# Kernel tuning notes

Measured on AMD Instinct MI355X. Metric: run time of the kernel, lower is better.

The kernel has to match this reference:

```python
import jax, jax.numpy as jnp
import numpy as np

B, S, V, E, P, C = 256, 128, 32000, 300, 200, 3
DIST_CUTOFF = 10

def _seq_mask(x):
    # TF: count_nonzero over seq, sequence_mask, expand to [B, S, 1]
    size = jnp.sum(x != 0, axis=1)
    m = (jnp.arange(S)[None, :] < size[:, None]).astype(jnp.float32)
    return m[:, :, None]

def _l2norm(w):
    n = jnp.sqrt(jnp.maximum(jnp.sum(w * w, axis=-1, keepdims=True), 1e-12))
    return w / n

def setup_inputs() -> dict:
    key = jax.random.key(0)
    ks = jax.random.split(key, 11)
    std = 0.01
    x1 = jax.random.randint(ks[0], (B, S), 0, V, dtype=jnp.int32)
    x2 = jax.random.randint(ks[1], (B, S), 0, V, dtype=jnp.int32)
    emb = jax.random.normal(ks[2], (V, E), jnp.float32)
    w_intra = jax.random.normal(ks[3], (E, E), jnp.float32) * std
    bias_intra = jax.random.normal(ks[4], (1,), jnp.float32) * std
    w_proj1 = jax.random.normal(ks[5], (2 * E, P), jnp.float32) * std
    w_proj2 = jax.random.normal(ks[6], (2 * E, P), jnp.float32) * std
    w_att = jax.random.normal(ks[7], (P, P), jnp.float32) * std
    w_cmp1 = jax.random.normal(ks[8], (2 * P, 2 * P), jnp.float32) * std
    w_cmp2 = jax.random.normal(ks[9], (2 * P, 2 * P), jnp.float32) * std
    w_agg = jax.random.normal(ks[10], (4 * P, C), jnp.float32) * std
    return dict(x1=x1, x2=x2, emb=emb, w_intra=w_intra, bias_intra=bias_intra,
                w_proj1=w_proj1, w_proj2=w_proj2, w_att=w_att,
                w_cmp1=w_cmp1, w_cmp2=w_cmp2, w_agg=w_agg)

def reference(x1, x2, emb, w_intra, bias_intra, w_proj1, w_proj2, w_att, w_cmp1, w_cmp2, w_agg):
    relu = jax.nn.relu
    mask1, mask2 = _seq_mask(x1), _seq_mask(x2)  # [B,S,1]

    # normalized embedding lookup
    e = _l2norm(emb)
    e1, e2 = e[x1], e[x2]  # [B,S,E]

    # intra-attention with distance bias (bias zeroed for |i-j| < 10)
    idx = jnp.arange(S)
    dist = jnp.abs(idx[None, :] - idx[:, None])
    dbias = bias_intra[0] * (dist >= DIST_CUTOFF).astype(jnp.float32)  # [S,S]

    def intra(x):
        f = relu(x @ w_intra)                       # shared F, [B,S,E]
        att = jnp.einsum('bik,bjk->bij', f, f)      # [B,S,S]
        sm = jax.nn.softmax(att + dbias[None], axis=2)
        xp = jnp.einsum('bik,bkj->bij', sm, x)
        return jnp.concatenate([x, xp], axis=2)     # [B,S,2E]

    e1, e2 = intra(e1), intra(e2)

    # project
    x1p = relu(e1 @ w_proj1)  # [B,S,P]
    x2p = relu(e2 @ w_proj2)

    # attend: F(x1) . F(x2), multiplicative mask, two softmaxes
    f1 = relu(x1p @ w_att)
    f2 = relu(x2p @ w_att)
    sim = jnp.einsum('bik,bjk->bij', f1, f2)          # [B,S1,S2]
    sim = sim * (mask1 * jnp.swapaxes(mask2, 1, 2))   # multiplicative mask (as in source)
    alpha = jnp.einsum('bki,bkj->bij', jax.nn.softmax(sim, axis=1), x1p)  # [B,S2,P]
    beta = jnp.einsum('bik,bkj->bij', jax.nn.softmax(sim, axis=2), x2p)   # [B,S1,P]

    # compare
    v1 = relu(jnp.concatenate([x1p, beta], axis=2) @ w_cmp1)
    v2 = relu(jnp.concatenate([x2p, alpha], axis=2) @ w_cmp2)

    # aggregate (masked sum pooling) + final ReLU projection (faithful to source)
    v1 = jnp.sum(v1 * mask1, axis=1)
    v2 = jnp.sum(v2 * mask2, axis=1)
    y_hat = relu(jnp.concatenate([v1, v2], axis=1) @ w_agg)  # [B,C]
    return y_hat
```

## Files before the change

kernel.cpp:

```cpp
#include <hip/hip_runtime.h>

#define BATCH 256
#define SEQ   128
#define EDIM  300
#define PDIM  200
#define BSTOK (BATCH * SEQ)

#define F_RELU  1
#define F_ACCUM 2

typedef unsigned short u16;
typedef __attribute__((ext_vector_type(8))) short bf16x8;
typedef __attribute__((ext_vector_type(4))) float f32x4;

__device__ __forceinline__ u16 f2bf(float x) {
    unsigned u = __float_as_uint(x);
    unsigned r = u + 0x7fffu + ((u >> 16) & 1u);
    return (u16)(r >> 16);
}
__device__ __forceinline__ float bf2f(u16 h) {
    return __uint_as_float(((unsigned)h) << 16);
}

__device__ __forceinline__ unsigned char* swz16(unsigned char* base, int row, int chunk) {
    return base + row * 64 + (((chunk ^ (row >> 1)) & 3) << 4);
}

__device__ __forceinline__ void split_store_swz(const float* va,
    unsigned char* bH, unsigned char* bL, int row, int c0)
{
    unsigned hp[8], lp[8];
    #pragma unroll
    for (int i = 0; i < 8; i++) {
        const unsigned u0 = __float_as_uint(va[2 * i]);
        const unsigned u1 = __float_as_uint(va[2 * i + 1]);
        const unsigned h0 = u0 & 0xffff0000u;
        const unsigned h1 = u1 & 0xffff0000u;
        hp[i] = (u0 >> 16) | h1;
        const float r0 = va[2 * i]     - __uint_as_float(h0);
        const float r1 = va[2 * i + 1] - __uint_as_float(h1);
        lp[i] = (__float_as_uint(r0) >> 16) | (__float_as_uint(r1) & 0xffff0000u);
    }
    *(uint4*)swz16(bH, row, c0)     = make_uint4(hp[0], hp[1], hp[2], hp[3]);
    *(uint4*)swz16(bH, row, c0 + 1) = make_uint4(hp[4], hp[5], hp[6], hp[7]);
    *(uint4*)swz16(bL, row, c0)     = make_uint4(lp[0], lp[1], lp[2], lp[3]);
    *(uint4*)swz16(bL, row, c0 + 1) = make_uint4(lp[4], lp[5], lp[6], lp[7]);
}

__device__ __forceinline__ void hi_store_swz(const float* va,
    unsigned char* bH, int row, int c0)
{
    unsigned hp[8];
    #pragma unroll
    for (int i = 0; i < 8; i++)
        hp[i] = (unsigned)f2bf(va[2 * i]) | ((unsigned)f2bf(va[2 * i + 1]) << 16);
    *(uint4*)swz16(bH, row, c0)     = make_uint4(hp[0], hp[1], hp[2], hp[3]);
    *(uint4*)swz16(bH, row, c0 + 1) = make_uint4(hp[4], hp[5], hp[6], hp[7]);
}

__device__ __forceinline__ void gload16(float* va, const float* __restrict__ src,
                                        bool row_ok)
{
    if (row_ok) {
        #pragma unroll
        for (int i = 0; i < 4; i++) {
            const float4 v = *(const float4*)(src + i * 4);
            va[i * 4 + 0] = v.x; va[i * 4 + 1] = v.y;
            va[i * 4 + 2] = v.z; va[i * 4 + 3] = v.w;
        }
    } else {
        #pragma unroll
        for (int i = 0; i < 16; i++) va[i] = 0.f;
    }
}

__device__ __forceinline__ void kmask16(float* va, int kbase, int Kvalid)
{
    #pragma unroll
    for (int i = 0; i < 16; i++)
        va[i] = (kbase + i < Kvalid) ? va[i] : 0.f;
}

__device__ __forceinline__ void gload_emb(float* va, const float* __restrict__ erow,
                                          int kb)
{
    if (kb + 16 <= EDIM) {
        #pragma unroll
        for (int i = 0; i < 4; i++) {
            const float4 v = *(const float4*)(erow + kb + i * 4);
            va[i * 4 + 0] = v.x; va[i * 4 + 1] = v.y;
            va[i * 4 + 2] = v.z; va[i * 4 + 3] = v.w;
        }
    } else {
        #pragma unroll
        for (int i = 0; i < 16; i++)
            va[i] = (kb + i < EDIM) ? erow[kb + i] : 0.f;
    }
}

#define MFMA3(ai, aj) \
    acc[ai][aj] = __builtin_amdgcn_mfma_f32_16x16x32_bf16(fah[ai], fbh[aj], acc[ai][aj], 0, 0, 0); \
    acc[ai][aj] = __builtin_amdgcn_mfma_f32_16x16x32_bf16(fah[ai], fbl[aj], acc[ai][aj], 0, 0, 0); \
    acc[ai][aj] = __builtin_amdgcn_mfma_f32_16x16x32_bf16(fal[ai], fbh[aj], acc[ai][aj], 0, 0, 0);

#define MFMA1(ai, aj) \
    acc[ai][aj] = __builtin_amdgcn_mfma_f32_16x16x32_bf16(fah[ai], fbh[aj], acc[ai][aj], 0, 0, 0);

__device__ __forceinline__ void store_transposed(
    float* __restrict__ PT, const f32x4 (*acc)[4], float* TR,
    int bn, int Nvalid, int wm, int wn, int lr, int quad, int tid, bool relu)
{
    #pragma unroll
    for (int h = 0; h < 2; h++) {
        __syncthreads();
        if ((wn >> 6) == h) {
            #pragma unroll
            for (int j = 0; j < 4; j++) {
                const int col = j * 16 + lr;
                #pragma unroll
                for (int i = 0; i < 4; i++)
                    #pragma unroll
                    for (int r = 0; r < 4; r++) {
                        float v = acc[i][j][r];
                        if (relu) v = fmaxf(v, 0.f);
                        TR[col * 129 + wm + i * 16 + quad * 4 + r] = v;
                    }
            }
        }
        __syncthreads();
        const int row = tid >> 2;
        const int gp = bn + h * 64 + row;
        if (gp < Nvalid) {
            float* dst = PT + (long long)gp * 128;
            for (int c = (tid & 3); c < 32; c += 4) {
                const int base = row * 129 + c * 4;
                *(float4*)(dst + c * 4) =
                    make_float4(TR[base], TR[base + 1], TR[base + 2], TR[base + 3]);
            }
        }
    }
}

__global__ __launch_bounds__(256) void gemm_proj(
    const int* __restrict__ x1, const int* __restrict__ x2,
    const float* __restrict__ emb, const float* __restrict__ norms,
    const u16* __restrict__ W1h, const u16* __restrict__ W1l,
    const u16* __restrict__ W2h, const u16* __restrict__ W2l,
    float* __restrict__ T, float* __restrict__ F0, float* __restrict__ F1)
{
    __shared__ __align__(16) unsigned char smem[65536];

    const int tid = threadIdx.x;
    const int id  = blockIdx.y * 5 + blockIdx.x;
    const int xcd = id & 7;
    const int s   = id >> 3;
    const int mt  = xcd + 8 * (s / 5);
    const int bm  = mt * 128;
    const int bn  = (s % 5) * 128;
    const bool side2 = mt >= 256;
    const bool wb = bn < 256;

    const u16* Bh = side2 ? W2h : W1h;
    const u16* Bl = side2 ? W2l : W1l;
    float* F = side2 ? F1 : F0;
    const int fm = side2 ? bm - 32768 : bm;
    const int* toks = (side2 ? x2 - 32768 : x1) + bm;

    const int wave = tid >> 6;
    const int lane = tid & 63;
    const int wm   = (wave >> 1) * 64;
    const int wn   = (wave & 1) * 64;
    const int lr   = lane & 15;
    const int quad = lane >> 4;
    const int sr   = tid >> 1;
    const int sc   = (tid & 1) * 16;
    const int c0   = (tid & 1) * 2;

    const int tok = toks[sr];
    const float nrm = norms[tok];
    const float* erow = emb + (long long)tok * EDIM;

    const int gn = bn + sr;
    const bool bok = gn < 556;
    const u16* Bhp = Bh + (long long)gn * 320 + sc;
    const u16* Blp = Bl + (long long)gn * 320 + sc;

    f32x4 acc[4][4];
    #pragma unroll
    for (int i = 0; i < 4; i++)
        #pragma unroll
        for (int j = 0; j < 4; j++)
            acc[i][j] = (f32x4)(0.0f);

    float av[16];
    uint4 bh0, bh1, bl0, bl1;

#define PROJ_LOAD(sidx) do { \
    const int kk_ = (sidx) * 32; \
    gload_emb(av, erow, kk_ + sc); \
    bh0 = bok ? *(const uint4*)(Bhp + kk_)     : make_uint4(0,0,0,0); \
    bh1 = bok ? *(const uint4*)(Bhp + kk_ + 8) : make_uint4(0,0,0,0); \
    if (wb) { \
        bl0 = bok ? *(const uint4*)(Blp + kk_)     : make_uint4(0,0,0,0); \
        bl1 = bok ? *(const uint4*)(Blp + kk_ + 8) : make_uint4(0,0,0,0); \
    } \
} while (0)

#define PROJ_COMMIT(bufp) do { \
    _Pragma("unroll") \
    for (int i_ = 0; i_ < 16; i_++) av[i_] *= nrm; \
    if (wb) split_store_swz(av, (bufp), (bufp) + 8192, sr, c0); \
    else    hi_store_swz(av, (bufp), sr, c0); \
    *(uint4*)swz16((bufp) + 16384, sr, c0)     = bh0; \
    *(uint4*)swz16((bufp) + 16384, sr, c0 + 1) = bh1; \
    if (wb) { \
        *(uint4*)swz16((bufp) + 24576, sr, c0)     = bl0; \
        *(uint4*)swz16((bufp) + 24576, sr, c0 + 1) = bl1; \
    } \
} while (0)

    PROJ_LOAD(0);
    PROJ_COMMIT(smem);
    PROJ_LOAD(1);
    __syncthreads();

    for (int t = 0; t < 10; ++t) {
        unsigned char* rb  = smem + (t & 1) * 32768;
        unsigned char* wbb = smem + ((t & 1) ^ 1) * 32768;

        bf16x8 fah[4], fbh[4];
        #pragma unroll
        for (int i = 0; i < 4; i++) {
            fah[i] = *(const bf16x8*)swz16(rb,         wm + i * 16 + lr, quad);
            fbh[i] = *(const bf16x8*)swz16(rb + 16384, wn + i * 16 + lr, quad);
        }
        if (wb) {
            bf16x8 fal[4], fbl[4];
            #pragma unroll
            for (int i = 0; i < 4; i++) {
                fal[i] = *(const bf16x8*)swz16(rb + 8192,  wm + i * 16 + lr, quad);
                fbl[i] = *(const bf16x8*)swz16(rb + 24576, wn + i * 16 + lr, quad);
            }
            if (t < 9) PROJ_COMMIT(wbb);
            if (t < 8) PROJ_LOAD(t + 2);
            #pragma unroll
            for (int i = 0; i < 4; i++)
                #pragma unroll
                for (int j = 0; j < 4; j++) { MFMA3(i, j) }
        } else {
            if (t < 9) PROJ_COMMIT(wbb);
            if (t < 8) PROJ_LOAD(t + 2);
            #pragma unroll
            for (int i = 0; i < 4; i++)
                #pragma unroll
                for (int j = 0; j < 4; j++) { MFMA1(i, j) }
        }
        __syncthreads();
    }
#undef PROJ_LOAD
#undef PROJ_COMMIT

    if (wb) {
        float* Tb = T + (long long)mt * (PDIM * SEQ);
        store_transposed(Tb, acc, (float*)smem, bn, PDIM, wm, wn, lr, quad, tid, false);
    } else {
        #pragma unroll
        for (int i = 0; i < 4; i++) {
            #pragma unroll
            for (int j = 0; j < 4; j++) {
                const int idx = bn + wn + j * 16 + lr - 256;
                if (idx >= EDIM) continue;
                #pragma unroll
                for (int r = 0; r < 4; r++) {
                    const int gm = fm + wm + i * 16 + quad * 4 + r;
                    F[(long long)gm * EDIM + idx] = fmaxf(acc[i][j][r], 0.f);
                }
            }
        }
    }
}

__global__ __launch_bounds__(256) void gemm_xp(
    const float* __restrict__ P, float* __restrict__ T,
    const int* __restrict__ x1, const int* __restrict__ x2,
    const float* __restrict__ emb, const float* __restrict__ norms,
    const u16* __restrict__ W1h, const u16* __restrict__ W1l,
    const u16* __restrict__ W2h, const u16* __restrict__ W2l,
    float* __restrict__ XCAT)
{
    __shared__ __align__(16) unsigned char smem[65536];

    const int tid = threadIdx.x;
    const int bz  = blockIdx.z;
    const int bn  = blockIdx.x * 128;

    const int wave = tid >> 6;
    const int lane = tid & 63;
    const int wm   = (wave >> 1) * 64;
    const int wn   = (wave & 1) * 64;
    const int lr   = lane & 15;
    const int quad = lane >> 4;
    const int sr   = tid >> 1;
    const int sc   = (tid & 1) * 16;
    const int c0   = (tid & 1) * 2;

    const int* toks = (bz < BATCH) ? x1 + bz * SEQ : x2 + (bz - BATCH) * SEQ;
    const u16* Wh = (bz < BATCH) ? W1h : W2h;
    const u16* Wl = (bz < BATCH) ? W1l : W2l;
    const int tok = toks[sr];
    const float nrm = norms[tok];
    const float* erow = emb + (long long)tok * EDIM;
    const float* Pb = P + (long long)bz * (SEQ * SEQ);
    float* Tb = T + (long long)bz * (PDIM * SEQ);

    const int gn = bn + sr;
    const bool bok = gn < PDIM;
    const u16* Whp = Wh + (long long)gn * 320 + sc;
    const u16* Wlp = Wl + (long long)gn * 320 + sc;
    const float* Pp = Pb + (long long)sr * 128 + sc;
    const float* Tp = Tb + (long long)gn * 128 + sc;

    f32x4 acc[4][4];
    #pragma unroll
    for (int i = 0; i < 4; i++)
        #pragma unroll
        for (int j = 0; j < 4; j++)
            acc[i][j] = (f32x4)(0.0f);

    float av[16], bv[16];
    uint4 bh0, bh1, bl0, bl1;

#define XP_LOAD(sidx) do { \
    if ((sidx) < 10) { \
        const int kk_ = (sidx) * 32; \
        gload_emb(av, erow, kk_ + sc); \
        bh0 = bok ? *(const uint4*)(Whp + kk_)     : make_uint4(0,0,0,0); \
        bh1 = bok ? *(const uint4*)(Whp + kk_ + 8) : make_uint4(0,0,0,0); \
        bl0 = bok ? *(const uint4*)(Wlp + kk_)     : make_uint4(0,0,0,0); \
        bl1 = bok ? *(const uint4*)(Wlp + kk_ + 8) : make_uint4(0,0,0,0); \
    } else { \
        const int kk_ = ((sidx) - 10) * 32; \
        gload16(av, Pp + kk_, true); \
        gload16(bv, Tp + kk_, bok); \
    } \
} while (0)

#define XP_COMMIT(sidx, bufp) do { \
    if ((sidx) < 10) { \
        _Pragma("unroll") \
        for (int i_ = 0; i_ < 16; i_++) av[i_] *= nrm; \
        split_store_swz(av, (bufp), (bufp) + 8192, sr, c0); \
        *(uint4*)swz16((bufp) + 16384, sr, c0)     = bh0; \
        *(uint4*)swz16((bufp) + 16384, sr, c0 + 1) = bh1; \
        *(uint4*)swz16((bufp) + 24576, sr, c0)     = bl0; \
        *(uint4*)swz16((bufp) + 24576, sr, c0 + 1) = bl1; \
    } else { \
        split_store_swz(av, (bufp),         (bufp) + 8192,  sr, c0); \
        split_store_swz(bv, (bufp) + 16384, (bufp) + 24576, sr, c0); \
    } \
} while (0)

    XP_LOAD(0);
    XP_COMMIT(0, smem);
    XP_LOAD(1);
    __syncthreads();

    for (int t = 0; t < 14; ++t) {
        unsigned char* rb  = smem + (t & 1) * 32768;
        unsigned char* wbb = smem + ((t & 1) ^ 1) * 32768;

        bf16x8 fah[4], fal[4], fbh[4], fbl[4];
        #pragma unroll
        for (int i = 0; i < 4; i++) {
            fah[i] = *(const bf16x8*)swz16(rb,         wm + i * 16 + lr, quad);
            fal[i] = *(const bf16x8*)swz16(rb + 8192,  wm + i * 16 + lr, quad);
            fbh[i] = *(const bf16x8*)swz16(rb + 16384, wn + i * 16 + lr, quad);
            fbl[i] = *(const bf16x8*)swz16(rb + 24576, wn + i * 16 + lr, quad);
        }
        if (t < 13) XP_COMMIT(t + 1, wbb);
        if (t < 12) XP_LOAD(t + 2);
        #pragma unroll
        for (int i = 0; i < 4; i++)
            #pragma unroll
            for (int j = 0; j < 4; j++) { MFMA3(i, j) }
        __syncthreads();
    }
#undef XP_LOAD
#undef XP_COMMIT

    const long long rowbase = (long long)bz * SEQ;
    #pragma unroll
    for (int i = 0; i < 4; i++) {
        #pragma unroll
        for (int j = 0; j < 4; j++) {
            const int gnn = bn + wn + j * 16 + lr;
            if (gnn >= PDIM) continue;
            #pragma unroll
            for (int r = 0; r < 4; r++) {
                const int gm = wm + i * 16 + quad * 4 + r;
                XCAT[(rowbase + gm) * 400 + gnn] = fmaxf(acc[i][j][r], 0.f);
            }
        }
    }
    store_transposed(Tb, acc, (float*)smem, bn, PDIM, wm, wn, lr, quad, tid, true);
}

template <int NM>
__global__ __launch_bounds__(256) void gemm_flat(
    const float* __restrict__ A,
    const u16* __restrict__ Bh, const u16* __restrict__ Bl,
    const u16* __restrict__ Bh2, const u16* __restrict__ Bl2, int Msplit,
    float* __restrict__ C, float* __restrict__ PO, const int* __restrict__ sizes,
    int M, int N, int Kp, int lda, int ldb, int ldc, int flags)
{
    constexpr int BUFB = (NM == 3) ? 32768 : 16384;
    constexpr int BOFF = (NM == 3) ? 16384 : 8192;
    __shared__ __align__(16) unsigned char smem[2 * BUFB];

    const int tid = threadIdx.x;
    int bx = blockIdx.x, by = blockIdx.y;
    if ((gridDim.y & 7) == 0) {
        const int gx = gridDim.x;
        const int id = by * gx + bx;
        const int xcd = id & 7;
        const int s = id >> 3;
        by = xcd + 8 * (s / gx);
        bx = s % gx;
    }
    const int bm = by * 128;
    const int bn = bx * 128;

    const int wave = tid >> 6;
    const int lane = tid & 63;
    const int wm   = (wave >> 1) * 64;
    const int wn   = (wave & 1) * 64;
    const int lr   = lane & 15;
    const int quad = lane >> 4;
    const int sr   = tid >> 1;
    const int sc   = (tid & 1) * 16;
    const int c0   = (tid & 1) * 2;

    if (bm >= Msplit) { Bh = Bh2; Bl = Bl2; }

    const float* Ap = A + (long long)(bm + sr) * lda + sc;
    const int gn = bn + sr;
    const bool bok = gn < N;
    const u16* Bhp = Bh + (long long)gn * ldb + sc;
    const u16* Blp = Bl + (long long)gn * ldb + sc;

    f32x4 acc[4][4];
    #pragma unroll
    for (int i = 0; i < 4; i++)
        #pragma unroll
        for (int j = 0; j < 4; j++)
            acc[i][j] = (f32x4)(0.0f);

    float av[16];
    uint4 bh0, bh1, bl0, bl1;

#define FLAT_LOAD(sidx) do { \
    const int kk_ = (sidx) * 32; \
    gload16(av, Ap + kk_, true); \
    bh0 = bok ? *(const uint4*)(Bhp + kk_)     : make_uint4(0,0,0,0); \
    bh1 = bok ? *(const uint4*)(Bhp + kk_ + 8) : make_uint4(0,0,0,0); \
    if constexpr (NM == 3) { \
        bl0 = bok ? *(const uint4*)(Blp + kk_)     : make_uint4(0,0,0,0); \
        bl1 = bok ? *(const uint4*)(Blp + kk_ + 8) : make_uint4(0,0,0,0); \
    } \
} while (0)

#define FLAT_COMMIT(bufp) do { \
    if constexpr (NM == 3) { \
        split_store_swz(av, (bufp), (bufp) + 8192, sr, c0); \
        *(uint4*)swz16((bufp) + BOFF + 8192, sr, c0)     = bl0; \
        *(uint4*)swz16((bufp) + BOFF + 8192, sr, c0 + 1) = bl1; \
    } else { \
        hi_store_swz(av, (bufp), sr, c0); \
    } \
    *(uint4*)swz16((bufp) + BOFF, sr, c0)     = bh0; \
    *(uint4*)swz16((bufp) + BOFF, sr, c0 + 1) = bh1; \
} while (0)

    const int NT = Kp >> 5;
    FLAT_LOAD(0);
    FLAT_COMMIT(smem);
    FLAT_LOAD(1);
    __syncthreads();

    for (int t = 0; t < NT; ++t) {
        unsigned char* rb  = smem + (t & 1) * BUFB;
        unsigned char* wbb = smem + ((t & 1) ^ 1) * BUFB;

        bf16x8 fah[4], fbh[4];
        #pragma unroll
        for (int i = 0; i < 4; i++) {
            fah[i] = *(const bf16x8*)swz16(rb,        wm + i * 16 + lr, quad);
            fbh[i] = *(const bf16x8*)swz16(rb + BOFF, wn + i * 16 + lr, quad);
        }
        if constexpr (NM == 3) {
            bf16x8 fal[4], fbl[4];
            #pragma unroll
            for (int i = 0; i < 4; i++) {
                fal[i] = *(const bf16x8*)swz16(rb + 8192,        wm + i * 16 + lr, quad);
                fbl[i] = *(const bf16x8*)swz16(rb + BOFF + 8192, wn + i * 16 + lr, quad);
            }
            if (t < NT - 1) FLAT_COMMIT(wbb);
            if (t < NT - 2) FLAT_LOAD(t + 2);
            #pragma unroll
            for (int i = 0; i < 4; i++)
                #pragma unroll
                for (int j = 0; j < 4; j++) { MFMA3(i, j) }
        } else {
            if (t < NT - 1) FLAT_COMMIT(wbb);
            if (t < NT - 2) FLAT_LOAD(t + 2);
            #pragma unroll
            for (int i = 0; i < 4; i++)
                #pragma unroll
                for (int j = 0; j < 4; j++) { MFMA1(i, j) }
        }
        __syncthreads();
    }
#undef FLAT_LOAD
#undef FLAT_COMMIT

    const int sz = PO ? sizes[bm >> 7] : 0;
    float ps[4] = {0.f, 0.f, 0.f, 0.f};
    #pragma unroll
    for (int j = 0; j < 4; j++) {
        const int gnn = bn + wn + j * 16 + lr;
        const bool gok = gnn < N;
        #pragma unroll
        for (int i = 0; i < 4; i++) {
            #pragma unroll
            for (int r = 0; r < 4; r++) {
                const int row = wm + i * 16 + quad * 4 + r;
                const int gm = bm + row;
                float v = acc[i][j][r];
                if (flags & F_RELU) v = fmaxf(v, 0.f);
                if (gok && C) C[(long long)gm * ldc + gnn] = v;
                if (PO && row < sz) ps[j] += v;
            }
        }
    }
    if (PO) {
        #pragma unroll
        for (int j = 0; j < 4; j++) {
            ps[j] += __shfl_xor(ps[j], 16);
            ps[j] += __shfl_xor(ps[j], 32);
        }
        float* PS = (float*)smem;
        __syncthreads();
        if (wm == 0 && quad == 0) {
            #pragma unroll
            for (int j = 0; j < 4; j++) PS[wn + j * 16 + lr] = ps[j];
        }
        __syncthreads();
        if (wm == 64 && quad == 0) {
            #pragma unroll
            for (int j = 0; j < 4; j++) PS[wn + j * 16 + lr] += ps[j];
        }
        __syncthreads();
        if (tid < 128) {
            const int gnn = bn + tid;
            if (gnn < N) PO[(long long)(bm >> 7) * N + gnn] = PS[tid];
        }
    }
}

#define SLD 132
template <int MODE>
__global__ __launch_bounds__(256) void gemm_bat(
    const float* __restrict__ A, const float* __restrict__ Aalt,
    const float* __restrict__ B, const float* __restrict__ Balt,
    float* __restrict__ C, float* __restrict__ PT,
    int N, int Kvalid, int Kp, int lda, int ldb, int ldc,
    long long sA, long long sB, long long sC, long long sPT,
    int flags, const float* __restrict__ bias_ptr, const int* __restrict__ sizes,
    int same_ab)
{
    constexpr int NM = (MODE == 0) ? 3 : 1;
    constexpr int BUFB = (NM == 3) ? 32768 : 16384;
    constexpr int BOFF = (NM == 3) ? 16384 : 8192;
    constexpr int SMB  = (MODE == 0) ? 65536 : (128 * SLD * 4);
    __shared__ __align__(16) unsigned char smem[SMB];

    const int bz = blockIdx.z;
    long long zb = bz;
    const float* Ause = A;
    const float* Buse = B;
    if (Aalt && bz >= BATCH) { Ause = Aalt; Buse = Balt; zb = bz - BATCH; }
    Ause += zb * sA;
    Buse += zb * sB;
    C += (long long)bz * sC;
    if (PT) PT += (long long)bz * sPT;

    const int tid  = threadIdx.x;
    const int bn   = blockIdx.x * 128;
    const int wave = tid >> 6;
    const int lane = tid & 63;
    const int wm   = (wave >> 1) * 64;
    const int wn   = (wave & 1) * 64;
    const int lr   = lane & 15;
    const int quad = lane >> 4;
    const int sr   = tid >> 1;
    const int sc   = (tid & 1) * 16;
    const int c0   = (tid & 1) * 2;

    f32x4 acc[4][4];
    #pragma unroll
    for (int i = 0; i < 4; i++)
        #pragma unroll
        for (int j = 0; j < 4; j++)
            acc[i][j] = (f32x4)(0.0f);

    const float* Apt = Ause + (long long)sr * lda + sc;
    const int gn = bn + sr;
    const bool bok = gn < N;
    const float* Bpt = Buse + (long long)gn * ldb + sc;

    float av[16], bv[16];

#define BAT_LOAD(sidx) do { \
    const int kk_ = (sidx) * 32; \
    gload16(av, Apt + kk_, true); \
    if (!same_ab) gload16(bv, Bpt + kk_, bok); \
} while (0)

#define BAT_COMMIT(sidx, bufp) do { \
    kmask16(av, (sidx) * 32 + sc, Kvalid); \
    if constexpr (NM == 3) split_store_swz(av, (bufp), (bufp) + 8192, sr, c0); \
    else                   hi_store_swz(av, (bufp), sr, c0); \
    if (!same_ab) { \
        kmask16(bv, (sidx) * 32 + sc, Kvalid); \
        if constexpr (NM == 3) \
            split_store_swz(bv, (bufp) + BOFF, (bufp) + BOFF + 8192, sr, c0); \
        else \
            hi_store_swz(bv, (bufp) + BOFF, sr, c0); \
    } \
} while (0)

    const int NT = Kp >> 5;
    BAT_LOAD(0);
    BAT_COMMIT(0, smem);
    BAT_LOAD(1);
    __syncthreads();

    for (int t = 0; t < NT; ++t) {
        unsigned char* rb  = smem + (t & 1) * BUFB;
        unsigned char* wbb = smem + ((t & 1) ^ 1) * BUFB;
        unsigned char* rbB = same_ab ? rb : rb + BOFF;

        bf16x8 fah[4], fbh[4];
        #pragma unroll
        for (int i = 0; i < 4; i++) {
            fah[i] = *(const bf16x8*)swz16(rb,  wm + i * 16 + lr, quad);
            fbh[i] = *(const bf16x8*)swz16(rbB, wn + i * 16 + lr, quad);
        }
        if constexpr (NM == 3) {
            bf16x8 fal[4], fbl[4];
            #pragma unroll
            for (int i = 0; i < 4; i++) {
                fal[i] = *(const bf16x8*)swz16(rb + 8192,  wm + i * 16 + lr, quad);
                fbl[i] = *(const bf16x8*)swz16(rbB + 8192, wn + i * 16 + lr, quad);
            }
            if (t < NT - 1) BAT_COMMIT(t + 1, wbb);
            if (t < NT - 2) BAT_LOAD(t + 2);
            #pragma unroll
            for (int i = 0; i < 4; i++)
                #pragma unroll
                for (int j = 0; j < 4; j++) { MFMA3(i, j) }
        } else {
            if (t < NT - 1) BAT_COMMIT(t + 1, wbb);
            if (t < NT - 2) BAT_LOAD(t + 2);
            #pragma unroll
            for (int i = 0; i < 4; i++)
                #pragma unroll
                for (int j = 0; j < 4; j++) { MFMA1(i, j) }
        }
        __syncthreads();
    }
#undef BAT_LOAD
#undef BAT_COMMIT

    if (MODE == 1) {
        float* S = (float*)smem;
        const float bias = bias_ptr[0];
        #pragma unroll
        for (int i = 0; i < 4; i++) {
            #pragma unroll
            for (int j = 0; j < 4; j++) {
                const int col = wn + j * 16 + lr;
                #pragma unroll
                for (int r = 0; r < 4; r++) {
                    const int row = wm + i * 16 + quad * 4 + r;
                    int d = row - col; d = d < 0 ? -d : d;
                    S[row * SLD + col] = acc[i][j][r] + ((d >= 10) ? bias : 0.f);
                }
            }
        }
        __syncthreads();
        const int row = tid >> 1;
        const int half = (tid & 1) * 64;
        float* Sr = S + row * SLD + half;
        float mx = -1e30f;
        #pragma unroll
        for (int c = 0; c < 16; c++) {
            const float4 v = *(const float4*)(Sr + c * 4);
            mx = fmaxf(fmaxf(fmaxf(mx, v.x), fmaxf(v.y, v.z)), v.w);
        }
        mx = fmaxf(mx, __shfl_xor(mx, 1));
        float sum = 0.f;
        #pragma unroll
        for (int c = 0; c < 16; c++) {
            float4 v = *(const float4*)(Sr + c * 4);
            v.x = __expf(v.x - mx); v.y = __expf(v.y - mx);
            v.z = __expf(v.z - mx); v.w = __expf(v.w - mx);
            sum += (v.x + v.y) + (v.z + v.w);
            *(float4*)(Sr + c * 4) = v;
        }
        sum += __shfl_xor(sum, 1);
        const float inv = 1.f / sum;
        #pragma unroll
        for (int c = 0; c < 16; c++) {
            float4 v = *(const float4*)(Sr + c * 4);
            v.x *= inv; v.y *= inv; v.z *= inv; v.w *= inv;
            *(float4*)&C[(long long)row * ldc + half + c * 4] = v;
        }
    } else if (MODE == 2) {
        float* S = (float*)smem;
        const int s1 = sizes[bz];
        const int s2 = sizes[BATCH + bz];
        #pragma unroll
        for (int i = 0; i < 4; i++) {
            #pragma unroll
            for (int j = 0; j < 4; j++) {
                const int col = wn + j * 16 + lr;
                #pragma unroll
                for (int r = 0; r < 4; r++) {
                    const int row = wm + i * 16 + quad * 4 + r;
                    float v = acc[i][j][r];
                    if (row >= s1 || col >= s2) v = 0.f;
                    S[row * SLD + col] = v;
                }
            }
        }
        __syncthreads();
        const int idx = tid >> 1;
        const int half = (tid & 1) * 64;
        {
            const float* Sr = S + idx * SLD + half;
            float mx = -1e30f;
            #pragma unroll
            for (int c = 0; c < 16; c++) {
                const float4 v = *(const float4*)(Sr + c * 4);
                mx = fmaxf(fmaxf(fmaxf(mx, v.x), fmaxf(v.y, v.z)), v.w);
            }
            mx = fmaxf(mx, __shfl_xor(mx, 1));
            float sum = 0.f;
            #pragma unroll
            for (int c = 0; c < 16; c++) {
                const float4 v = *(const float4*)(Sr + c * 4);
                sum += (__expf(v.x - mx) + __expf(v.y - mx))
                     + (__expf(v.z - mx) + __expf(v.w - mx));
            }
            sum += __shfl_xor(sum, 1);
            const float inv = 1.f / sum;
            #pragma unroll
            for (int c = 0; c < 16; c++) {
                const float4 v = *(const float4*)(Sr + c * 4);
                float4 o;
                o.x = __expf(v.x - mx) * inv; o.y = __expf(v.y - mx) * inv;
                o.z = __expf(v.z - mx) * inv; o.w = __expf(v.w - mx) * inv;
                *(float4*)&C[(long long)idx * 128 + half + c * 4] = o;
            }
        }
        {
            float mx = -1e30f;
            for (int r = 0; r < 64; r++)
                mx = fmaxf(mx, S[(half + r) * SLD + idx]);
            mx = fmaxf(mx, __shfl_xor(mx, 1));
            float sum = 0.f;
            for (int r = 0; r < 64; r++)
                sum += __expf(S[(half + r) * SLD + idx] - mx);
            sum += __shfl_xor(sum, 1);
            const float inv = 1.f / sum;
            #pragma unroll
            for (int r4 = 0; r4 < 16; r4++) {
                float4 o;
                o.x = __expf(S[(half + r4 * 4 + 0) * SLD + idx] - mx) * inv;
                o.y = __expf(S[(half + r4 * 4 + 1) * SLD + idx] - mx) * inv;
                o.z = __expf(S[(half + r4 * 4 + 2) * SLD + idx] - mx) * inv;
                o.w = __expf(S[(half + r4 * 4 + 3) * SLD + idx] - mx) * inv;
                *(float4*)&PT[(long long)idx * 128 + half + r4 * 4] = o;
            }
        }
    } else {
        const int s1 = sizes ? sizes[bz] : SEQ;
        const int s2 = sizes ? sizes[BATCH + bz] : SEQ;
        #pragma unroll
        for (int i = 0; i < 4; i++) {
            #pragma unroll
            for (int j = 0; j < 4; j++) {
                const int gnn = bn + wn + j * 16 + lr;
                if (gnn >= N) continue;
                #pragma unroll
                for (int r = 0; r < 4; r++) {
                    const int gm = wm + i * 16 + quad * 4 + r;
                    float v = acc[i][j][r];
                    if (sizes && (gm >= s1 || gnn >= s2)) v = 0.f;
                    if (flags & F_ACCUM) v += C[(long long)gm * ldc + gnn];
                    if (flags & F_RELU)  v = fmaxf(v, 0.f);
                    C[(long long)gm * ldc + gnn] = v;
                    if (PT) PT[(long long)gnn * 128 + gm] = v;
                }
            }
        }
    }
}

struct WEnt { const float* src; u16* H; u16* L; int K, N, Kp, rowStart; };
struct WTab { WEnt e[11]; };
__global__ void convert_all(WTab t)
{
    const int row = blockIdx.y;
    const int k = blockIdx.x * 256 + threadIdx.x;
    #pragma unroll
    for (int s = 0; s < 11; s++) {
        const WEnt w = t.e[s];
        if (row >= w.rowStart && row < w.rowStart + w.N) {
            const int n = row - w.rowStart;
            if (k < w.Kp) {
                const float v = (k < w.K) ? w.src[(long long)k * w.N + n] : 0.f;
                const u16 h = f2bf(v);
                w.H[(long long)n * w.Kp + k] = h;
                w.L[(long long)n * w.Kp + k] = f2bf(v - bf2f(h));
            }
            return;
        }
    }
}

__global__ void norms_kernel(const float* __restrict__ emb, float* __restrict__ norms)
{
    const int r = blockIdx.x;
    const int lane = threadIdx.x;
    const float* row = emb + (long long)r * EDIM;
    float ss = 0.f;
    #pragma unroll
    for (int i = 0; i < 5; i++) {
        const int c = lane + i * 64;
        const float f = (c < EDIM) ? row[c] : 0.f;
        ss += f * f;
    }
    #pragma unroll
    for (int o = 32; o > 0; o >>= 1) ss += __shfl_xor(ss, o);
    if (lane == 0) norms[r] = rsqrtf(fmaxf(ss, 1e-12f));
}

__global__ void sizes_kernel(const int* __restrict__ x1, const int* __restrict__ x2,
                             int* __restrict__ sizes)
{
    const int b = blockIdx.x;
    const int side = blockIdx.y;
    const int* x = (side ? x2 : x1) + b * SEQ;
    const int nz = (x[threadIdx.x] != 0) ? 1 : 0;
    const unsigned long long bal = __ballot(nz);
    __shared__ int part[2];
    if ((threadIdx.x & 63) == 0) part[threadIdx.x >> 6] = __popcll(bal);
    __syncthreads();
    if (threadIdx.x == 0) sizes[side * BATCH + b] = part[0] + part[1];
}

__global__ void agg_kernel(const float* __restrict__ v1s, const float* __restrict__ v2s,
                           const float* __restrict__ w_agg, float* __restrict__ y)
{
    const int b = blockIdx.x;
    const int lane = threadIdx.x;
    float a0 = 0.f, a1 = 0.f, a2 = 0.f;
    for (int k = lane; k < 800; k += 64) {
        const float v = (k < 400) ? v1s[b * 400 + k] : v2s[b * 400 + k - 400];
        a0 = fmaf(v, w_agg[k * 3 + 0], a0);
        a1 = fmaf(v, w_agg[k * 3 + 1], a1);
        a2 = fmaf(v, w_agg[k * 3 + 2], a2);
    }
    #pragma unroll
    for (int o = 32; o > 0; o >>= 1) {
        a0 += __shfl_xor(a0, o);
        a1 += __shfl_xor(a1, o);
        a2 += __shfl_xor(a2, o);
    }
    if (lane == 0) {
        y[b * 3 + 0] = fmaxf(a0, 0.f);
        y[b * 3 + 1] = fmaxf(a1, 0.f);
        y[b * 3 + 2] = fmaxf(a2, 0.f);
    }
}

extern "C" void kernel_launch(void* const* d_in, const int* in_sizes, int n_in,
                              void* d_out, int out_size, void* d_ws, size_t ws_size,
                              hipStream_t stream)
{
    (void)in_sizes; (void)n_in; (void)out_size; (void)ws_size;
    const int*   x1         = (const int*)d_in[0];
    const int*   x2         = (const int*)d_in[1];
    const float* emb        = (const float*)d_in[2];
    const float* w_intra    = (const float*)d_in[3];
    const float* bias_intra = (const float*)d_in[4];
    const float* w_proj1    = (const float*)d_in[5];
    const float* w_proj2    = (const float*)d_in[6];
    const float* w_att      = (const float*)d_in[7];
    const float* w_cmp1     = (const float*)d_in[8];
    const float* w_cmp2     = (const float*)d_in[9];
    const float* w_agg      = (const float*)d_in[10];
    float* y  = (float*)d_out;
    float* ws = (float*)d_ws;

    float* X1CAT = ws;
    float* X2CAT = X1CAT + 13107200;
    float* T     = X2CAT + 13107200;
    float* FBUF  = T + 13107200;
    float* ATT   = FBUF + 9830400;
    float* POOL  = ATT + 8388608;
    int*   SIZES = (int*)(POOL + 204800);
    float* NORMS = (float*)(SIZES + 512);
    u16*   W1H   = (u16*)(NORMS + 32768);
    u16*   W1L   = W1H + 177920;
    u16*   W2H   = W1L + 177920;
    u16*   W2L   = W2H + 177920;
    u16*   WAH   = W2L + 177920;
    u16*   WAL   = WAH + 44800;
    u16*   WC1H  = WAL + 44800;
    u16*   WC1L  = WC1H + 166400;
    u16*   WC2H  = WC1L + 166400;
    u16*   WC2L  = WC2H + 166400;
    u16*   WPA1H = WC2L + 166400;
    u16*   WPA1L = WPA1H + 64000;
    u16*   WPA2H = WPA1L + 64000;
    u16*   WPA2L = WPA2H + 64000;

    float* F1X = X1CAT;
    float* F12 = FBUF;
    float* F2  = FBUF + 6553600;
    float* SIMP = F2;
    float* SMTP = F12;
    float* T1  = T;
    float* T2  = T + 6553600;

    const long long sbSS = (long long)SEQ * SEQ;
    const long long sbF  = (long long)SEQ * EDIM;
    const long long sbFP = 25600;
    const long long sbC  = (long long)SEQ * 400;
    const long long sbT  = (long long)PDIM * SEQ;

    sizes_kernel<<<dim3(BATCH, 2), 128, 0, stream>>>(x1, x2, SIZES);
    norms_kernel<<<32000, 64, 0, stream>>>(emb, NORMS);

    {
        WTab t;
        t.e[0]  = { w_proj1 + 300 * 200, W1H,             W1L,             300, 200, 320, 0    };
        t.e[1]  = { w_intra,             W1H + 200 * 320, W1L + 200 * 320,   0,  56, 320, 200  };
        t.e[2]  = { w_intra,             W1H + 256 * 320, W1L + 256 * 320, 300, 300, 320, 256  };
        t.e[3]  = { w_proj2 + 300 * 200, W2H,             W2L,             300, 200, 320, 556  };
        t.e[4]  = { w_intra,             W2H + 200 * 320, W2L + 200 * 320,   0,  56, 320, 756  };
        t.e[5]  = { w_intra,             W2H + 256 * 320, W2L + 256 * 320, 300, 300, 320, 812  };
        t.e[6]  = { w_att,               WAH,             WAL,             200, 200, 224, 1112 };
        t.e[7]  = { w_cmp1,              WC1H,            WC1L,            400, 400, 416, 1312 };
        t.e[8]  = { w_cmp2,              WC2H,            WC2L,            400, 400, 416, 1712 };
        t.e[9]  = { w_proj1,             WPA1H,           WPA1L,           300, 200, 320, 2112 };
        t.e[10] = { w_proj2,             WPA2H,           WPA2L,           300, 200, 320, 2312 };
        convert_all<<<dim3(2, 2512), 256, 0, stream>>>(t);
    }

    gemm_proj<<<dim3(5, 512), 256, 0, stream>>>(
        x1, x2, emb, NORMS, W1H, W1L, W2H, W2L, T, FBUF, F1X);
    gemm_bat<1><<<dim3(1, 1, 2 * BATCH), 256, 0, stream>>>(
        FBUF, F1X, FBUF, nullptr, ATT, nullptr,
        SEQ, EDIM, 320, EDIM, EDIM, SEQ, sbF, sbF, sbSS, 0,
        0, bias_intra, nullptr, 1);
    gemm_xp<<<dim3(2, 1, 2 * BATCH), 256, 0, stream>>>(
        ATT, T, x1, x2, emb, NORMS, WPA1H, WPA1L, WPA2H, WPA2L, X1CAT);

    gemm_flat<1><<<dim3(2, 512), 256, 0, stream>>>(
        X1CAT, WAH, WAL, WAH, WAL, 1 << 30, F12, nullptr, nullptr,
        2 * BSTOK, PDIM, 224, 400, 224, PDIM, F_RELU);
    gemm_bat<2><<<dim3(1, 1, BATCH), 256, 0, stream>>>(
        F12, nullptr, F2, nullptr, SIMP, SMTP,
        SEQ, PDIM, 224, PDIM, PDIM, SEQ, sbFP, sbFP, sbFP, sbFP,
        0, nullptr, SIZES, 0);
    gemm_bat<0><<<dim3(2, 1, 2 * BATCH), 256, 0, stream>>>(
        SIMP, SMTP, T2, T1, X1CAT + 200, nullptr,
        PDIM, SEQ, SEQ, SEQ, SEQ, 400, sbFP, sbT, sbC, 0,
        0, nullptr, nullptr, 0);

    gemm_flat<3><<<dim3(4, 512), 256, 0, stream>>>(
        X1CAT, WC1H, WC1L, WC2H, WC2L, BSTOK,
        nullptr, POOL, SIZES,
        2 * BSTOK, 400, 416, 400, 416, 400, F_RELU);
    agg_kernel<<<BATCH, 64, 0, stream>>>(POOL, POOL + 102400, w_agg, y);
}
```

Measured before the change: 555.2 us.

## Use 512-thread blocks with single-buffered LDS across all GEMM kernels

Every GEMM kernel moves from 256 to 512 threads per block, with 8 waves each owning a 64x32 sub-tile instead of 4 waves owning 64x64. The LDS double-buffering and register prefetch pipeline is removed in favour of a single 32 KB buffer loaded each k-step, which halves shared memory and accumulator registers per thread. Softmax epilogues are re-partitioned to four threads per row with extra shuffles. The intent is higher occupancy and more waves to hide latency, at the cost of losing the load/compute overlap and adding a barrier per k-step.

```diff
diff --git a/kernel.cpp b/kernel.cpp
--- a/kernel.cpp
+++ b/kernel.cpp
@@ -26,12 +26,12 @@
     return base + row * 64 + (((chunk ^ (row >> 1)) & 3) << 4);
 }
 
-__device__ __forceinline__ void split_store_swz(const float* va,
-    unsigned char* bH, unsigned char* bL, int row, int c0)
-{
-    unsigned hp[8], lp[8];
-    #pragma unroll
-    for (int i = 0; i < 8; i++) {
+__device__ __forceinline__ void split_store8(const float* va,
+    unsigned char* bH, unsigned char* bL, int row, int chunk)
+{
+    unsigned hp[4], lp[4];
+    #pragma unroll
+    for (int i = 0; i < 4; i++) {
         const unsigned u0 = __float_as_uint(va[2 * i]);
         const unsigned u1 = __float_as_uint(va[2 * i + 1]);
         const unsigned h0 = u0 & 0xffff0000u;
@@ -41,61 +41,56 @@
         const float r1 = va[2 * i + 1] - __uint_as_float(h1);
         lp[i] = (__float_as_uint(r0) >> 16) | (__float_as_uint(r1) & 0xffff0000u);
     }
-    *(uint4*)swz16(bH, row, c0)     = make_uint4(hp[0], hp[1], hp[2], hp[3]);
-    *(uint4*)swz16(bH, row, c0 + 1) = make_uint4(hp[4], hp[5], hp[6], hp[7]);
-    *(uint4*)swz16(bL, row, c0)     = make_uint4(lp[0], lp[1], lp[2], lp[3]);
-    *(uint4*)swz16(bL, row, c0 + 1) = make_uint4(lp[4], lp[5], lp[6], lp[7]);
-}
-
-__device__ __forceinline__ void hi_store_swz(const float* va,
-    unsigned char* bH, int row, int c0)
-{
-    unsigned hp[8];
+    *(uint4*)swz16(bH, row, chunk) = make_uint4(hp[0], hp[1], hp[2], hp[3]);
+    *(uint4*)swz16(bL, row, chunk) = make_uint4(lp[0], lp[1], lp[2], lp[3]);
+}
+
+__device__ __forceinline__ void hi_store8(const float* va,
+    unsigned char* bH, int row, int chunk)
+{
+    unsigned hp[4];
+    #pragma unroll
+    for (int i = 0; i < 4; i++)
+        hp[i] = (unsigned)f2bf(va[2 * i]) | ((unsigned)f2bf(va[2 * i + 1]) << 16);
+    *(uint4*)swz16(bH, row, chunk) = make_uint4(hp[0], hp[1], hp[2], hp[3]);
+}
+
+__device__ __forceinline__ void gload8(float* va, const float* __restrict__ src,
+                                       bool ok)
+{
+    if (ok) {
+        const float4 v0 = *(const float4*)(src);
+        const float4 v1 = *(const float4*)(src + 4);
+        va[0] = v0.x; va[1] = v0.y; va[2] = v0.z; va[3] = v0.w;
+        va[4] = v1.x; va[5] = v1.y; va[6] = v1.z; va[7] = v1.w;
+    } else {
+        #pragma unroll
+        for (int i = 0; i < 8; i++) va[i] = 0.f;
+    }
+}
+
+__device__ __forceinline__ void kmask8(float* va, int kbase, int Kvalid)
+{
     #pragma unroll
     for (int i = 0; i < 8; i++)
-        hp[i] = (unsigned)f2bf(va[2 * i]) | ((unsigned)f2bf(va[2 * i + 1]) << 16);
-    *(uint4*)swz16(bH, row, c0)     = make_uint4(hp[0], hp[1], hp[2], hp[3]);
-    *(uint4*)swz16(bH, row, c0 + 1) = make_uint4(hp[4], hp[5], hp[6], hp[7]);
-}
-
-__device__ __forceinline__ void gload16(float* va, const float* __restrict__ src,
-                                        bool row_ok)
-{
-    if (row_ok) {
-        #pragma unroll
-        for (int i = 0; i < 4; i++) {
-            const float4 v = *(const float4*)(src + i * 4);
-            va[i * 4 + 0] = v.x; va[i * 4 + 1] = v.y;
-            va[i * 4 + 2] = v.z; va[i * 4 + 3] = v.w;
-        }
+        va[i] = (kbase + i < Kvalid) ? va[i] : 0.f;
+}
+
+__device__ __forceinline__ void gather8(float* va, const float* __restrict__ erow,
+                                        float nrm, int kb)
+{
+    if (kb + 8 <= EDIM) {
+        const float4 v0 = *(const float4*)(erow + kb);
+        const float4 v1 = *(const float4*)(erow + kb + 4);
+        va[0] = v0.x; va[1] = v0.y; va[2] = v0.z; va[3] = v0.w;
+        va[4] = v1.x; va[5] = v1.y; va[6] = v1.z; va[7] = v1.w;
     } else {
         #pragma unroll
-        for (int i = 0; i < 16; i++) va[i] = 0.f;
-    }
-}
-
-__device__ __forceinline__ void kmask16(float* va, int kbase, int Kvalid)
-{
-    #pragma unroll
-    for (int i = 0; i < 16; i++)
-        va[i] = (kbase + i < Kvalid) ? va[i] : 0.f;
-}
-
-__device__ __forceinline__ void gload_emb(float* va, const float* __restrict__ erow,
-                                          int kb)
-{
-    if (kb + 16 <= EDIM) {
-        #pragma unroll
-        for (int i = 0; i < 4; i++) {
-            const float4 v = *(const float4*)(erow + kb + i * 4);
-            va[i * 4 + 0] = v.x; va[i * 4 + 1] = v.y;
-            va[i * 4 + 2] = v.z; va[i * 4 + 3] = v.w;
-        }
-    } else {
-        #pragma unroll
-        for (int i = 0; i < 16; i++)
+        for (int i = 0; i < 8; i++)
             va[i] = (kb + i < EDIM) ? erow[kb + i] : 0.f;
     }
+    #pragma unroll
+    for (int i = 0; i < 8; i++) va[i] *= nrm;
 }
 
 #define MFMA3(ai, aj) \
@@ -106,33 +101,34 @@
 #define MFMA1(ai, aj) \
     acc[ai][aj] = __builtin_amdgcn_mfma_f32_16x16x32_bf16(fah[ai], fbh[aj], acc[ai][aj], 0, 0, 0);
 
+
 __device__ __forceinline__ void store_transposed(
-    float* __restrict__ PT, const f32x4 (*acc)[4], float* TR,
-    int bn, int Nvalid, int wm, int wn, int lr, int quad, int tid, bool relu)
+    float* __restrict__ PT, const f32x4 (*acc)[2], float* TR,
+    int bn, int Nvalid, int wr, int wc, int lr, int quad, int tid, bool relu)
 {
     #pragma unroll
     for (int h = 0; h < 2; h++) {
         __syncthreads();
-        if ((wn >> 6) == h) {
-            #pragma unroll
-            for (int j = 0; j < 4; j++) {
-                const int col = j * 16 + lr;
+        if ((wc >> 6) == h) {
+            #pragma unroll
+            for (int j = 0; j < 2; j++) {
+                const int col = (wc & 63) + j * 16 + lr;
                 #pragma unroll
                 for (int i = 0; i < 4; i++)
                     #pragma unroll
                     for (int r = 0; r < 4; r++) {
                         float v = acc[i][j][r];
                         if (relu) v = fmaxf(v, 0.f);
-                        TR[col * 129 + wm + i * 16 + quad * 4 + r] = v;
+                        TR[col * 129 + wr + i * 16 + quad * 4 + r] = v;
                     }
             }
         }
         __syncthreads();
-        const int row = tid >> 2;
+        const int row = tid >> 3;
         const int gp = bn + h * 64 + row;
         if (gp < Nvalid) {
             float* dst = PT + (long long)gp * 128;
-            for (int c = (tid & 3); c < 32; c += 4) {
+            for (int c = (tid & 7); c < 32; c += 8) {
                 const int base = row * 129 + c * 4;
                 *(float4*)(dst + c * 4) =
                     make_float4(TR[base], TR[base + 1], TR[base + 2], TR[base + 3]);
@@ -141,14 +137,14 @@
     }
 }
 
-__global__ __launch_bounds__(256) void gemm_proj(
+__global__ __launch_bounds__(512, 4) void gemm_proj(
     const int* __restrict__ x1, const int* __restrict__ x2,
     const float* __restrict__ emb, const float* __restrict__ norms,
     const u16* __restrict__ W1h, const u16* __restrict__ W1l,
     const u16* __restrict__ W2h, const u16* __restrict__ W2l,
     float* __restrict__ T, float* __restrict__ F0, float* __restrict__ F1)
 {
-    __shared__ __align__(16) unsigned char smem[65536];
+    __shared__ __align__(16) unsigned char smem[33280];
 
     const int tid = threadIdx.x;
     const int id  = blockIdx.y * 5 + blockIdx.x;
@@ -168,13 +164,13 @@
 
     const int wave = tid >> 6;
     const int lane = tid & 63;
-    const int wm   = (wave >> 1) * 64;
-    const int wn   = (wave & 1) * 64;
+    const int wr   = (wave >> 2) * 64;
+    const int wc   = (wave & 3) * 32;
     const int lr   = lane & 15;
     const int quad = lane >> 4;
-    const int sr   = tid >> 1;
-    const int sc   = (tid & 1) * 16;
-    const int c0   = (tid & 1) * 2;
+    const int sr   = tid >> 2;
+    const int q    = tid & 3;
+    const int scf  = q * 8;
 
     const int tok = toks[sr];
     const float nrm = norms[tok];
@@ -182,97 +178,72 @@
 
     const int gn = bn + sr;
     const bool bok = gn < 556;
-    const u16* Bhp = Bh + (long long)gn * 320 + sc;
-    const u16* Blp = Bl + (long long)gn * 320 + sc;
-
-    f32x4 acc[4][4];
+    const u16* Bhp = Bh + (long long)gn * 320 + scf;
+    const u16* Blp = Bl + (long long)gn * 320 + scf;
+
+    f32x4 acc[4][2];
     #pragma unroll
     for (int i = 0; i < 4; i++)
         #pragma unroll
-        for (int j = 0; j < 4; j++)
+        for (int j = 0; j < 2; j++)
             acc[i][j] = (f32x4)(0.0f);
 
-    float av[16];
-    uint4 bh0, bh1, bl0, bl1;
-
-#define PROJ_LOAD(sidx) do { \
-    const int kk_ = (sidx) * 32; \
-    gload_emb(av, erow, kk_ + sc); \
-    bh0 = bok ? *(const uint4*)(Bhp + kk_)     : make_uint4(0,0,0,0); \
-    bh1 = bok ? *(const uint4*)(Bhp + kk_ + 8) : make_uint4(0,0,0,0); \
-    if (wb) { \
-        bl0 = bok ? *(const uint4*)(Blp + kk_)     : make_uint4(0,0,0,0); \
-        bl1 = bok ? *(const uint4*)(Blp + kk_ + 8) : make_uint4(0,0,0,0); \
-    } \
-} while (0)
-
-#define PROJ_COMMIT(bufp) do { \
-    _Pragma("unroll") \
-    for (int i_ = 0; i_ < 16; i_++) av[i_] *= nrm; \
-    if (wb) split_store_swz(av, (bufp), (bufp) + 8192, sr, c0); \
-    else    hi_store_swz(av, (bufp), sr, c0); \
-    *(uint4*)swz16((bufp) + 16384, sr, c0)     = bh0; \
-    *(uint4*)swz16((bufp) + 16384, sr, c0 + 1) = bh1; \
-    if (wb) { \
-        *(uint4*)swz16((bufp) + 24576, sr, c0)     = bl0; \
-        *(uint4*)swz16((bufp) + 24576, sr, c0 + 1) = bl1; \
-    } \
-} while (0)
-
-    PROJ_LOAD(0);
-    PROJ_COMMIT(smem);
-    PROJ_LOAD(1);
-    __syncthreads();
-
     for (int t = 0; t < 10; ++t) {
-        unsigned char* rb  = smem + (t & 1) * 32768;
-        unsigned char* wbb = smem + ((t & 1) ^ 1) * 32768;
-
-        bf16x8 fah[4], fbh[4];
-        #pragma unroll
-        for (int i = 0; i < 4; i++) {
-            fah[i] = *(const bf16x8*)swz16(rb,         wm + i * 16 + lr, quad);
-            fbh[i] = *(const bf16x8*)swz16(rb + 16384, wn + i * 16 + lr, quad);
-        }
+        float av[8];
+        gather8(av, erow, nrm, t * 32 + scf);
+        const uint4 bh = bok ? *(const uint4*)(Bhp + t * 32) : make_uint4(0,0,0,0);
         if (wb) {
-            bf16x8 fal[4], fbl[4];
-            #pragma unroll
-            for (int i = 0; i < 4; i++) {
-                fal[i] = *(const bf16x8*)swz16(rb + 8192,  wm + i * 16 + lr, quad);
-                fbl[i] = *(const bf16x8*)swz16(rb + 24576, wn + i * 16 + lr, quad);
-            }
-            if (t < 9) PROJ_COMMIT(wbb);
-            if (t < 8) PROJ_LOAD(t + 2);
+            const uint4 bl = bok ? *(const uint4*)(Blp + t * 32) : make_uint4(0,0,0,0);
+            split_store8(av, smem, smem + 8192, sr, q);
+            *(uint4*)swz16(smem + 16384, sr, q) = bh;
+            *(uint4*)swz16(smem + 24576, sr, q) = bl;
+        } else {
+            hi_store8(av, smem, sr, q);
+            *(uint4*)swz16(smem + 16384, sr, q) = bh;
+        }
+        __syncthreads();
+
+        bf16x8 fah[4], fbh[2];
+        #pragma unroll
+        for (int i = 0; i < 4; i++)
+            fah[i] = *(const bf16x8*)swz16(smem, wr + i * 16 + lr, quad);
+        #pragma unroll
+        for (int j = 0; j < 2; j++)
+            fbh[j] = *(const bf16x8*)swz16(smem + 16384, wc + j * 16 + lr, quad);
+        if (wb) {
+            bf16x8 fal[4], fbl[2];
             #pragma unroll
             for (int i = 0; i < 4; i++)
-                #pragma unroll
-                for (int j = 0; j < 4; j++) { MFMA3(i, j) }
+                fal[i] = *(const bf16x8*)swz16(smem + 8192, wr + i * 16 + lr, quad);
+            #pragma unroll
+            for (int j = 0; j < 2; j++)
+                fbl[j] = *(const bf16x8*)swz16(smem + 24576, wc + j * 16 + lr, quad);
+            #pragma unroll
+            for (int i = 0; i < 4; i++)
+                #pragma unroll
+                for (int j = 0; j < 2; j++) { MFMA3(i, j) }
         } else {
-            if (t < 9) PROJ_COMMIT(wbb);
-            if (t < 8) PROJ_LOAD(t + 2);
             #pragma unroll
             for (int i = 0; i < 4; i++)
                 #pragma unroll
-                for (int j = 0; j < 4; j++) { MFMA1(i, j) }
-        }
-        __syncthreads();
-    }
-#undef PROJ_LOAD
-#undef PROJ_COMMIT
+                for (int j = 0; j < 2; j++) { MFMA1(i, j) }
+        }
+        __syncthreads();
+    }
 
     if (wb) {
         float* Tb = T + (long long)mt * (PDIM * SEQ);
-        store_transposed(Tb, acc, (float*)smem, bn, PDIM, wm, wn, lr, quad, tid, false);
+        store_transposed(Tb, acc, (float*)smem, bn, PDIM, wr, wc, lr, quad, tid, false);
     } else {
         #pragma unroll
         for (int i = 0; i < 4; i++) {
             #pragma unroll
-            for (int j = 0; j < 4; j++) {
-                const int idx = bn + wn + j * 16 + lr - 256;
+            for (int j = 0; j < 2; j++) {
+                const int idx = bn + wc + j * 16 + lr - 256;
                 if (idx >= EDIM) continue;
                 #pragma unroll
                 for (int r = 0; r < 4; r++) {
-                    const int gm = fm + wm + i * 16 + quad * 4 + r;
+                    const int gm = fm + wr + i * 16 + quad * 4 + r;
                     F[(long long)gm * EDIM + idx] = fmaxf(acc[i][j][r], 0.f);
                 }
             }
@@ -280,7 +251,7 @@
     }
 }
 
-__global__ __launch_bounds__(256) void gemm_xp(
+__global__ __launch_bounds__(512, 4) void gemm_xp(
     const float* __restrict__ P, float* __restrict__ T,
     const int* __restrict__ x1, const int* __restrict__ x2,
     const float* __restrict__ emb, const float* __restrict__ norms,
@@ -288,7 +259,7 @@
     const u16* __restrict__ W2h, const u16* __restrict__ W2l,
     float* __restrict__ XCAT)
 {
-    __shared__ __align__(16) unsigned char smem[65536];
+    __shared__ __align__(16) unsigned char smem[33280];
 
     const int tid = threadIdx.x;
     const int bz  = blockIdx.z;
@@ -296,13 +267,13 @@
 
     const int wave = tid >> 6;
     const int lane = tid & 63;
-    const int wm   = (wave >> 1) * 64;
-    const int wn   = (wave & 1) * 64;
+    const int wr   = (wave >> 2) * 64;
+    const int wc   = (wave & 3) * 32;
     const int lr   = lane & 15;
     const int quad = lane >> 4;
-    const int sr   = tid >> 1;
-    const int sc   = (tid & 1) * 16;
-    const int c0   = (tid & 1) * 2;
+    const int sr   = tid >> 2;
+    const int q    = tid & 3;
+    const int scf  = q * 8;
 
     const int* toks = (bz < BATCH) ? x1 + bz * SEQ : x2 + (bz - BATCH) * SEQ;
     const u16* Wh = (bz < BATCH) ? W1h : W2h;
@@ -315,107 +286,81 @@
 
     const int gn = bn + sr;
     const bool bok = gn < PDIM;
-    const u16* Whp = Wh + (long long)gn * 320 + sc;
-    const u16* Wlp = Wl + (long long)gn * 320 + sc;
-    const float* Pp = Pb + (long long)sr * 128 + sc;
-    const float* Tp = Tb + (long long)gn * 128 + sc;
-
-    f32x4 acc[4][4];
+    const u16* Whp = Wh + (long long)gn * 320 + scf;
+    const u16* Wlp = Wl + (long long)gn * 320 + scf;
+    const float* Pp = Pb + (long long)sr * 128 + scf;
+    const float* Tp = Tb + (long long)gn * 128 + scf;
+
+    f32x4 acc[4][2];
     #pragma unroll
     for (int i = 0; i < 4; i++)
         #pragma unroll
-        for (int j = 0; j < 4; j++)
+        for (int j = 0; j < 2; j++)
             acc[i][j] = (f32x4)(0.0f);
 
-    float av[16], bv[16];
-    uint4 bh0, bh1, bl0, bl1;
-
-#define XP_LOAD(sidx) do { \
-    if ((sidx) < 10) { \
-        const int kk_ = (sidx) * 32; \
-        gload_emb(av, erow, kk_ + sc); \
-        bh0 = bok ? *(const uint4*)(Whp + kk_)     : make_uint4(0,0,0,0); \
-        bh1 = bok ? *(const uint4*)(Whp + kk_ + 8) : make_uint4(0,0,0,0); \
-        bl0 = bok ? *(const uint4*)(Wlp + kk_)     : make_uint4(0,0,0,0); \
-        bl1 = bok ? *(const uint4*)(Wlp + kk_ + 8) : make_uint4(0,0,0,0); \
-    } else { \
-        const int kk_ = ((sidx) - 10) * 32; \
-        gload16(av, Pp + kk_, true); \
-        gload16(bv, Tp + kk_, bok); \
-    } \
-} while (0)
-
-#define XP_COMMIT(sidx, bufp) do { \
-    if ((sidx) < 10) { \
-        _Pragma("unroll") \
-        for (int i_ = 0; i_ < 16; i_++) av[i_] *= nrm; \
-        split_store_swz(av, (bufp), (bufp) + 8192, sr, c0); \
-        *(uint4*)swz16((bufp) + 16384, sr, c0)     = bh0; \
-        *(uint4*)swz16((bufp) + 16384, sr, c0 + 1) = bh1; \
-        *(uint4*)swz16((bufp) + 24576, sr, c0)     = bl0; \
-        *(uint4*)swz16((bufp) + 24576, sr, c0 + 1) = bl1; \
-    } else { \
-        split_store_swz(av, (bufp),         (bufp) + 8192,  sr, c0); \
-        split_store_swz(bv, (bufp) + 16384, (bufp) + 24576, sr, c0); \
-    } \
-} while (0)
-
-    XP_LOAD(0);
-    XP_COMMIT(0, smem);
-    XP_LOAD(1);
-    __syncthreads();
-
     for (int t = 0; t < 14; ++t) {
-        unsigned char* rb  = smem + (t & 1) * 32768;
-        unsigned char* wbb = smem + ((t & 1) ^ 1) * 32768;
-
-        bf16x8 fah[4], fal[4], fbh[4], fbl[4];
+        if (t < 10) {
+            float av[8];
+            gather8(av, erow, nrm, t * 32 + scf);
+            const uint4 bh = bok ? *(const uint4*)(Whp + t * 32) : make_uint4(0,0,0,0);
+            const uint4 bl = bok ? *(const uint4*)(Wlp + t * 32) : make_uint4(0,0,0,0);
+            split_store8(av, smem, smem + 8192, sr, q);
+            *(uint4*)swz16(smem + 16384, sr, q) = bh;
+            *(uint4*)swz16(smem + 24576, sr, q) = bl;
+        } else {
+            float av[8], bv[8];
+            gload8(av, Pp + (t - 10) * 32, true);
+            gload8(bv, Tp + (t - 10) * 32, bok);
+            split_store8(av, smem,         smem + 8192,  sr, q);
+            split_store8(bv, smem + 16384, smem + 24576, sr, q);
+        }
+        __syncthreads();
+
+        bf16x8 fah[4], fal[4], fbh[2], fbl[2];
         #pragma unroll
         for (int i = 0; i < 4; i++) {
-            fah[i] = *(const bf16x8*)swz16(rb,         wm + i * 16 + lr, quad);
-            fal[i] = *(const bf16x8*)swz16(rb + 8192,  wm + i * 16 + lr, quad);
-            fbh[i] = *(const bf16x8*)swz16(rb + 16384, wn + i * 16 + lr, quad);
-            fbl[i] = *(const bf16x8*)swz16(rb + 24576, wn + i * 16 + lr, quad);
-        }
-        if (t < 13) XP_COMMIT(t + 1, wbb);
-        if (t < 12) XP_LOAD(t + 2);
+            fah[i] = *(const bf16x8*)swz16(smem,        wr + i * 16 + lr, quad);
+            fal[i] = *(const bf16x8*)swz16(smem + 8192, wr + i * 16 + lr, quad);
+        }
+        #pragma unroll
+        for (int j = 0; j < 2; j++) {
+            fbh[j] = *(const bf16x8*)swz16(smem + 16384, wc + j * 16 + lr, quad);
+            fbl[j] = *(const bf16x8*)swz16(smem + 24576, wc + j * 16 + lr, quad);
+        }
         #pragma unroll
         for (int i = 0; i < 4; i++)
             #pragma unroll
-            for (int j = 0; j < 4; j++) { MFMA3(i, j) }
-        __syncthreads();
-    }
-#undef XP_LOAD
-#undef XP_COMMIT
+            for (int j = 0; j < 2; j++) { MFMA3(i, j) }
+        __syncthreads();
+    }
 
     const long long rowbase = (long long)bz * SEQ;
     #pragma unroll
     for (int i = 0; i < 4; i++) {
         #pragma unroll
-        for (int j = 0; j < 4; j++) {
-            const int gnn = bn + wn + j * 16 + lr;
+        for (int j = 0; j < 2; j++) {
+            const int gnn = bn + wc + j * 16 + lr;
             if (gnn >= PDIM) continue;
             #pragma unroll
             for (int r = 0; r < 4; r++) {
-                const int gm = wm + i * 16 + quad * 4 + r;
+                const int gm = wr + i * 16 + quad * 4 + r;
                 XCAT[(rowbase + gm) * 400 + gnn] = fmaxf(acc[i][j][r], 0.f);
             }
         }
     }
-    store_transposed(Tb, acc, (float*)smem, bn, PDIM, wm, wn, lr, quad, tid, true);
+    store_transposed(Tb, acc, (float*)smem, bn, PDIM, wr, wc, lr, quad, tid, true);
 }
 
 template <int NM>
-__global__ __launch_bounds__(256) void gemm_flat(
+__global__ __launch_bounds__(512, 4) void gemm_flat(
     const float* __restrict__ A,
     const u16* __restrict__ Bh, const u16* __restrict__ Bl,
     const u16* __restrict__ Bh2, const u16* __restrict__ Bl2, int Msplit,
     float* __restrict__ C, float* __restrict__ PO, const int* __restrict__ sizes,
     int M, int N, int Kp, int lda, int ldb, int ldc, int flags)
 {
-    constexpr int BUFB = (NM == 3) ? 32768 : 16384;
     constexpr int BOFF = (NM == 3) ? 16384 : 8192;
-    __shared__ __align__(16) unsigned char smem[2 * BUFB];
+    __shared__ __align__(16) unsigned char smem[(NM == 3) ? 32768 : 16384];
 
     const int tid = threadIdx.x;
     int bx = blockIdx.x, by = blockIdx.y;
@@ -432,108 +377,84 @@
 
     const int wave = tid >> 6;
     const int lane = tid & 63;
-    const int wm   = (wave >> 1) * 64;
-    const int wn   = (wave & 1) * 64;
+    const int wr   = (wave >> 2) * 64;
+    const int wc   = (wave & 3) * 32;
     const int lr   = lane & 15;
     const int quad = lane >> 4;
-    const int sr   = tid >> 1;
-    const int sc   = (tid & 1) * 16;
-    const int c0   = (tid & 1) * 2;
+    const int sr   = tid >> 2;
+    const int q    = tid & 3;
+    const int scf  = q * 8;
 
     if (bm >= Msplit) { Bh = Bh2; Bl = Bl2; }
 
-    const float* Ap = A + (long long)(bm + sr) * lda + sc;
+    const float* Ap = A + (long long)(bm + sr) * lda + scf;
     const int gn = bn + sr;
     const bool bok = gn < N;
-    const u16* Bhp = Bh + (long long)gn * ldb + sc;
-    const u16* Blp = Bl + (long long)gn * ldb + sc;
-
-    f32x4 acc[4][4];
+    const u16* Bhp = Bh + (long long)gn * ldb + scf;
+    const u16* Blp = Bl + (long long)gn * ldb + scf;
+
+    f32x4 acc[4][2];
     #pragma unroll
     for (int i = 0; i < 4; i++)
         #pragma unroll
-        for (int j = 0; j < 4; j++)
+        for (int j = 0; j < 2; j++)
             acc[i][j] = (f32x4)(0.0f);
 
-    float av[16];
-    uint4 bh0, bh1, bl0, bl1;
-
-#define FLAT_LOAD(sidx) do { \
-    const int kk_ = (sidx) * 32; \
-    gload16(av, Ap + kk_, true); \
-    bh0 = bok ? *(const uint4*)(Bhp + kk_)     : make_uint4(0,0,0,0); \
-    bh1 = bok ? *(const uint4*)(Bhp + kk_ + 8) : make_uint4(0,0,0,0); \
-    if constexpr (NM == 3) { \
-        bl0 = bok ? *(const uint4*)(Blp + kk_)     : make_uint4(0,0,0,0); \
-        bl1 = bok ? *(const uint4*)(Blp + kk_ + 8) : make_uint4(0,0,0,0); \
-    } \
-} while (0)
-
-#define FLAT_COMMIT(bufp) do { \
-    if constexpr (NM == 3) { \
-        split_store_swz(av, (bufp), (bufp) + 8192, sr, c0); \
-        *(uint4*)swz16((bufp) + BOFF + 8192, sr, c0)     = bl0; \
-        *(uint4*)swz16((bufp) + BOFF + 8192, sr, c0 + 1) = bl1; \
-    } else { \
-        hi_store_swz(av, (bufp), sr, c0); \
-    } \
-    *(uint4*)swz16((bufp) + BOFF, sr, c0)     = bh0; \
-    *(uint4*)swz16((bufp) + BOFF, sr, c0 + 1) = bh1; \
-} while (0)
-
     const int NT = Kp >> 5;
-    FLAT_LOAD(0);
-    FLAT_COMMIT(smem);
-    FLAT_LOAD(1);
-    __syncthreads();
-
     for (int t = 0; t < NT; ++t) {
-        unsigned char* rb  = smem + (t & 1) * BUFB;
-        unsigned char* wbb = smem + ((t & 1) ^ 1) * BUFB;
-
-        bf16x8 fah[4], fbh[4];
+        float av[8];
+        gload8(av, Ap + t * 32, true);
+        const uint4 bh = bok ? *(const uint4*)(Bhp + t * 32) : make_uint4(0,0,0,0);
+        if constexpr (NM == 3) {
+            const uint4 bl = bok ? *(const uint4*)(Blp + t * 32) : make_uint4(0,0,0,0);
+            split_store8(av, smem, smem + 8192, sr, q);
+            *(uint4*)swz16(smem + BOFF,        sr, q) = bh;
+            *(uint4*)swz16(smem + BOFF + 8192, sr, q) = bl;
+        } else {
+            hi_store8(av, smem, sr, q);
+            *(uint4*)swz16(smem + BOFF, sr, q) = bh;
+        }
+        __syncthreads();
+
+        bf16x8 fah[4], fbh[2];
+        #pragma unroll
+        for (int i = 0; i < 4; i++)
+            fah[i] = *(const bf16x8*)swz16(smem, wr + i * 16 + lr, quad);
+        #pragma unroll
+        for (int j = 0; j < 2; j++)
+            fbh[j] = *(const bf16x8*)swz16(smem + BOFF, wc + j * 16 + lr, quad);
+        if constexpr (NM == 3) {
+            bf16x8 fal[4], fbl[2];
+            #pragma unroll
+            for (int i = 0; i < 4; i++)
+                fal[i] = *(const bf16x8*)swz16(smem + 8192, wr + i * 16 + lr, quad);
+            #pragma unroll
+            for (int j = 0; j < 2; j++)
+                fbl[j] = *(const bf16x8*)swz16(smem + BOFF + 8192, wc + j * 16 + lr, quad);
+            #pragma unroll
+            for (int i = 0; i < 4; i++)
+                #pragma unroll
+                for (int j = 0; j < 2; j++) { MFMA3(i, j) }
+        } else {
+            #pragma unroll
+            for (int i = 0; i < 4; i++)
+                #pragma unroll
+                for (int j = 0; j < 2; j++) { MFMA1(i, j) }
+        }
+        __syncthreads();
+    }
+
+    const int sz = PO ? sizes[bm >> 7] : 0;
+    float ps[2] = {0.f, 0.f};
+    #pragma unroll
+    for (int j = 0; j < 2; j++) {
+        const int gnn = bn + wc + j * 16 + lr;
+        const bool gok = gnn < N;
         #pragma unroll
         for (int i = 0; i < 4; i++) {
-            fah[i] = *(const bf16x8*)swz16(rb,        wm + i * 16 + lr, quad);
-            fbh[i] = *(const bf16x8*)swz16(rb + BOFF, wn + i * 16 + lr, quad);
-        }
-        if constexpr (NM == 3) {
-            bf16x8 fal[4], fbl[4];
-            #pragma unroll
-            for (int i = 0; i < 4; i++) {
-                fal[i] = *(const bf16x8*)swz16(rb + 8192,        wm + i * 16 + lr, quad);
-                fbl[i] = *(const bf16x8*)swz16(rb + BOFF + 8192, wn + i * 16 + lr, quad);
-            }
-            if (t < NT - 1) FLAT_COMMIT(wbb);
-            if (t < NT - 2) FLAT_LOAD(t + 2);
-            #pragma unroll
-            for (int i = 0; i < 4; i++)
-                #pragma unroll
-                for (int j = 0; j < 4; j++) { MFMA3(i, j) }
-        } else {
-            if (t < NT - 1) FLAT_COMMIT(wbb);
-            if (t < NT - 2) FLAT_LOAD(t + 2);
-            #pragma unroll
-            for (int i = 0; i < 4; i++)
-                #pragma unroll
-                for (int j = 0; j < 4; j++) { MFMA1(i, j) }
-        }
-        __syncthreads();
-    }
-#undef FLAT_LOAD
-#undef FLAT_COMMIT
-
-    const int sz = PO ? sizes[bm >> 7] : 0;
-    float ps[4] = {0.f, 0.f, 0.f, 0.f};
-    #pragma unroll
-    for (int j = 0; j < 4; j++) {
-        const int gnn = bn + wn + j * 16 + lr;
-        const bool gok = gnn < N;
-        #pragma unroll
-        for (int i = 0; i < 4; i++) {
             #pragma unroll
             for (int r = 0; r < 4; r++) {
-                const int row = wm + i * 16 + quad * 4 + r;
+                const int row = wr + i * 16 + quad * 4 + r;
                 const int gm = bm + row;
                 float v = acc[i][j][r];
                 if (flags & F_RELU) v = fmaxf(v, 0.f);
@@ -544,20 +465,20 @@
     }
     if (PO) {
         #pragma unroll
-        for (int j = 0; j < 4; j++) {
+        for (int j = 0; j < 2; j++) {
             ps[j] += __shfl_xor(ps[j], 16);
             ps[j] += __shfl_xor(ps[j], 32);
         }
         float* PS = (float*)smem;
         __syncthreads();
-        if (wm == 0 && quad == 0) {
-            #pragma unroll
-            for (int j = 0; j < 4; j++) PS[wn + j * 16 + lr] = ps[j];
-        }
-        __syncthreads();
-        if (wm == 64 && quad == 0) {
-            #pragma unroll
-            for (int j = 0; j < 4; j++) PS[wn + j * 16 + lr] += ps[j];
+        if (wr == 0 && quad == 0) {
+            #pragma unroll
+            for (int j = 0; j < 2; j++) PS[wc + j * 16 + lr] = ps[j];
+        }
+        __syncthreads();
+        if (wr == 64 && quad == 0) {
+            #pragma unroll
+            for (int j = 0; j < 2; j++) PS[wc + j * 16 + lr] += ps[j];
         }
         __syncthreads();
         if (tid < 128) {
@@ -569,7 +490,7 @@
 
 #define SLD 132
 template <int MODE>
-__global__ __launch_bounds__(256) void gemm_bat(
+__global__ __launch_bounds__(512, (MODE == 0) ? 4 : 2) void gemm_bat(
     const float* __restrict__ A, const float* __restrict__ Aalt,
     const float* __restrict__ B, const float* __restrict__ Balt,
     float* __restrict__ C, float* __restrict__ PT,
@@ -579,9 +500,8 @@
     int same_ab)
 {
     constexpr int NM = (MODE == 0) ? 3 : 1;
-    constexpr int BUFB = (NM == 3) ? 32768 : 16384;
     constexpr int BOFF = (NM == 3) ? 16384 : 8192;
-    constexpr int SMB  = (MODE == 0) ? 65536 : (128 * SLD * 4);
+    constexpr int SMB  = (MODE == 0) ? 32768 : (128 * SLD * 4);
     __shared__ __align__(16) unsigned char smem[SMB];
 
     const int bz = blockIdx.z;
@@ -598,89 +518,70 @@
     const int bn   = blockIdx.x * 128;
     const int wave = tid >> 6;
     const int lane = tid & 63;
-    const int wm   = (wave >> 1) * 64;
-    const int wn   = (wave & 1) * 64;
+    const int wr   = (wave >> 2) * 64;
+    const int wc   = (wave & 3) * 32;
     const int lr   = lane & 15;
     const int quad = lane >> 4;
-    const int sr   = tid >> 1;
-    const int sc   = (tid & 1) * 16;
-    const int c0   = (tid & 1) * 2;
-
-    f32x4 acc[4][4];
+    const int sr   = tid >> 2;
+    const int q    = tid & 3;
+    const int scf  = q * 8;
+
+    f32x4 acc[4][2];
     #pragma unroll
     for (int i = 0; i < 4; i++)
         #pragma unroll
-        for (int j = 0; j < 4; j++)
+        for (int j = 0; j < 2; j++)
             acc[i][j] = (f32x4)(0.0f);
 
-    const float* Apt = Ause + (long long)sr * lda + sc;
+    const float* Apt = Ause + (long long)sr * lda + scf;
     const int gn = bn + sr;
     const bool bok = gn < N;
-    const float* Bpt = Buse + (long long)gn * ldb + sc;
-
-    float av[16], bv[16];
-
-#define BAT_LOAD(sidx) do { \
-    const int kk_ = (sidx) * 32; \
-    gload16(av, Apt + kk_, true); \
-    if (!same_ab) gload16(bv, Bpt + kk_, bok); \
-} while (0)
-
-#define BAT_COMMIT(sidx, bufp) do { \
-    kmask16(av, (sidx) * 32 + sc, Kvalid); \
-    if constexpr (NM == 3) split_store_swz(av, (bufp), (bufp) + 8192, sr, c0); \
-    else                   hi_store_swz(av, (bufp), sr, c0); \
-    if (!same_ab) { \
-        kmask16(bv, (sidx) * 32 + sc, Kvalid); \
-        if constexpr (NM == 3) \
-            split_store_swz(bv, (bufp) + BOFF, (bufp) + BOFF + 8192, sr, c0); \
-        else \
-            hi_store_swz(bv, (bufp) + BOFF, sr, c0); \
-    } \
-} while (0)
+    const float* Bpt = Buse + (long long)gn * ldb + scf;
 
     const int NT = Kp >> 5;
-    BAT_LOAD(0);
-    BAT_COMMIT(0, smem);
-    BAT_LOAD(1);
-    __syncthreads();
-
     for (int t = 0; t < NT; ++t) {
-        unsigned char* rb  = smem + (t & 1) * BUFB;
-        unsigned char* wbb = smem + ((t & 1) ^ 1) * BUFB;
-        unsigned char* rbB = same_ab ? rb : rb + BOFF;
-
-        bf16x8 fah[4], fbh[4];
-        #pragma unroll
-        for (int i = 0; i < 4; i++) {
-            fah[i] = *(const bf16x8*)swz16(rb,  wm + i * 16 + lr, quad);
-            fbh[i] = *(const bf16x8*)swz16(rbB, wn + i * 16 + lr, quad);
-        }
+        float av[8];
+        gload8(av, Apt + t * 32, true);
+        kmask8(av, t * 32 + scf, Kvalid);
+        if constexpr (NM == 3) split_store8(av, smem, smem + 8192, sr, q);
+        else                   hi_store8(av, smem, sr, q);
+        if (!same_ab) {
+            float bv[8];
+            gload8(bv, Bpt + t * 32, bok);
+            kmask8(bv, t * 32 + scf, Kvalid);
+            if constexpr (NM == 3) split_store8(bv, smem + BOFF, smem + BOFF + 8192, sr, q);
+            else                   hi_store8(bv, smem + BOFF, sr, q);
+        }
+        __syncthreads();
+
+        unsigned char* rbB = same_ab ? smem : smem + BOFF;
+        bf16x8 fah[4], fbh[2];
+        #pragma unroll
+        for (int i = 0; i < 4; i++)
+            fah[i] = *(const bf16x8*)swz16(smem, wr + i * 16 + lr, quad);
+        #pragma unroll
+        for (int j = 0; j < 2; j++)
+            fbh[j] = *(const bf16x8*)swz16(rbB, wc + j * 16 + lr, quad);
         if constexpr (NM == 3) {
-            bf16x8 fal[4], fbl[4];
-            #pragma unroll
-            for (int i = 0; i < 4; i++) {
-                fal[i] = *(const bf16x8*)swz16(rb + 8192,  wm + i * 16 + lr, quad);
-                fbl[i] = *(const bf16x8*)swz16(rbB + 8192, wn + i * 16 + lr, quad);
-            }
-            if (t < NT - 1) BAT_COMMIT(t + 1, wbb);
-            if (t < NT - 2) BAT_LOAD(t + 2);
+            bf16x8 fal[4], fbl[2];
             #pragma unroll
             for (int i = 0; i < 4; i++)
-                #pragma unroll
-                for (int j = 0; j < 4; j++) { MFMA3(i, j) }
+                fal[i] = *(const bf16x8*)swz16(smem + 8192, wr + i * 16 + lr, quad);
+            #pragma unroll
+            for (int j = 0; j < 2; j++)
+                fbl[j] = *(const bf16x8*)swz16(rbB + 8192, wc + j * 16 + lr, quad);
+            #pragma unroll
+            for (int i = 0; i < 4; i++)
+                #pragma unroll
+                for (int j = 0; j < 2; j++) { MFMA3(i, j) }
         } else {
-            if (t < NT - 1) BAT_COMMIT(t + 1, wbb);
-            if (t < NT - 2) BAT_LOAD(t + 2);
             #pragma unroll
             for (int i = 0; i < 4; i++)
                 #pragma unroll
-                for (int j = 0; j < 4; j++) { MFMA1(i, j) }
-        }
-        __syncthreads();
-    }
-#undef BAT_LOAD
-#undef BAT_COMMIT
+                for (int j = 0; j < 2; j++) { MFMA1(i, j) }
+        }
+        __syncthreads();
+    }
 
     if (MODE == 1) {
         float* S = (float*)smem;
@@ -688,30 +589,31 @@
         #pragma unroll
         for (int i = 0; i < 4; i++) {
             #pragma unroll
-            for (int j = 0; j < 4; j++) {
-                const int col = wn + j * 16 + lr;
+            for (int j = 0; j < 2; j++) {
+                const int col = wc + j * 16 + lr;
                 #pragma unroll
                 for (int r = 0; r < 4; r++) {
-                    const int row = wm + i * 16 + quad * 4 + r;
+                    const int row = wr + i * 16 + quad * 4 + r;
                     int d = row - col; d = d < 0 ? -d : d;
                     S[row * SLD + col] = acc[i][j][r] + ((d >= 10) ? bias : 0.f);
                 }
             }
         }
         __syncthreads();
-        const int row = tid >> 1;
-        const int half = (tid & 1) * 64;
-        float* Sr = S + row * SLD + half;
+        const int row = tid >> 2;
+        const int qd  = (tid & 3) * 32;
+        float* Sr = S + row * SLD + qd;
         float mx = -1e30f;
         #pragma unroll
-        for (int c = 0; c < 16; c++) {
+        for (int c = 0; c < 8; c++) {
             const float4 v = *(const float4*)(Sr + c * 4);
             mx = fmaxf(fmaxf(fmaxf(mx, v.x), fmaxf(v.y, v.z)), v.w);
         }
         mx = fmaxf(mx, __shfl_xor(mx, 1));
+        mx = fmaxf(mx, __shfl_xor(mx, 2));
         float sum = 0.f;
         #pragma unroll
-        for (int c = 0; c < 16; c++) {
+        for (int c = 0; c < 8; c++) {
             float4 v = *(const float4*)(Sr + c * 4);
             v.x = __expf(v.x - mx); v.y = __expf(v.y - mx);
             v.z = __expf(v.z - mx); v.w = __expf(v.w - mx);
@@ -719,12 +621,13 @@
             *(float4*)(Sr + c * 4) = v;
         }
         sum += __shfl_xor(sum, 1);
+        sum += __shfl_xor(sum, 2);
         const float inv = 1.f / sum;
         #pragma unroll
-        for (int c = 0; c < 16; c++) {
+        for (int c = 0; c < 8; c++) {
             float4 v = *(const float4*)(Sr + c * 4);
             v.x *= inv; v.y *= inv; v.z *= inv; v.w *= inv;
-            *(float4*)&C[(long long)row * ldc + half + c * 4] = v;
+            *(float4*)&C[(long long)row * ldc + qd + c * 4] = v;
         }
     } else if (MODE == 2) {
         float* S = (float*)smem;
@@ -733,11 +636,11 @@
         #pragma unroll
         for (int i = 0; i < 4; i++) {
             #pragma unroll
-            for (int j = 0; j < 4; j++) {
-                const int col = wn + j * 16 + lr;
+            for (int j = 0; j < 2; j++) {
+                const int col = wc + j * 16 + lr;
                 #pragma unroll
                 for (int r = 0; r < 4; r++) {
-                    const int row = wm + i * 16 + quad * 4 + r;
+                    const int row = wr + i * 16 + quad * 4 + r;
                     float v = acc[i][j][r];
                     if (row >= s1 || col >= s2) v = 0.f;
                     S[row * SLD + col] = v;
@@ -745,53 +648,58 @@
             }
         }
         __syncthreads();
-        const int idx = tid >> 1;
-        const int half = (tid & 1) * 64;
+        const int row = tid >> 2;
+        const int qd  = (tid & 3) * 32;
         {
-            const float* Sr = S + idx * SLD + half;
+            const float* Sr = S + row * SLD + qd;
             float mx = -1e30f;
             #pragma unroll
-            for (int c = 0; c < 16; c++) {
+            for (int c = 0; c < 8; c++) {
                 const float4 v = *(const float4*)(Sr + c * 4);
                 mx = fmaxf(fmaxf(fmaxf(mx, v.x), fmaxf(v.y, v.z)), v.w);
             }
             mx = fmaxf(mx, __shfl_xor(mx, 1));
+            mx = fmaxf(mx, __shfl_xor(mx, 2));
             float sum = 0.f;
             #pragma unroll
-            for (int c = 0; c < 16; c++) {
+            for (int c = 0; c < 8; c++) {
                 const float4 v = *(const float4*)(Sr + c * 4);
                 sum += (__expf(v.x - mx) + __expf(v.y - mx))
                      + (__expf(v.z - mx) + __expf(v.w - mx));
             }
             sum += __shfl_xor(sum, 1);
+            sum += __shfl_xor(sum, 2);
             const float inv = 1.f / sum;
             #pragma unroll
-            for (int c = 0; c < 16; c++) {
+            for (int c = 0; c < 8; c++) {
                 const float4 v = *(const float4*)(Sr + c * 4);
                 float4 o;
                 o.x = __expf(v.x - mx) * inv; o.y = __expf(v.y - mx) * inv;
                 o.z = __expf(v.z - mx) * inv; o.w = __expf(v.w - mx) * inv;
-                *(float4*)&C[(long long)idx * 128 + half + c * 4] = o;
+                *(float4*)&C[(long long)row * 128 + qd + c * 4] = o;
             }
         }
         {
+            const int colx = row;
             float mx = -1e30f;
-            for (int r = 0; r < 64; r++)
-                mx = fmaxf(mx, S[(half + r) * SLD + idx]);
+            for (int r = 0; r < 32; r++)
+                mx = fmaxf(mx, S[(qd + r) * SLD + colx]);
             mx = fmaxf(mx, __shfl_xor(mx, 1));
+            mx = fmaxf(mx, __shfl_xor(mx, 2));
             float sum = 0.f;
-            for (int r = 0; r < 64; r++)
-                sum += __expf(S[(half + r) * SLD + idx] - mx);
+            for (int r = 0; r < 32; r++)
+                sum += __expf(S[(qd + r) * SLD + colx] - mx);
             sum += __shfl_xor(sum, 1);
+            sum += __shfl_xor(sum, 2);
             const float inv = 1.f / sum;
             #pragma unroll
-            for (int r4 = 0; r4 < 16; r4++) {
+            for (int r4 = 0; r4 < 8; r4++) {
                 float4 o;
-                o.x = __expf(S[(half + r4 * 4 + 0) * SLD + idx] - mx) * inv;
-                o.y = __expf(S[(half + r4 * 4 + 1) * SLD + idx] - mx) * inv;
-                o.z = __expf(S[(half + r4 * 4 + 2) * SLD + idx] - mx) * inv;
-                o.w = __expf(S[(half + r4 * 4 + 3) * SLD + idx] - mx) * inv;
-                *(float4*)&PT[(long long)idx * 128 + half + r4 * 4] = o;
+                o.x = __expf(S[(qd + r4 * 4 + 0) * SLD + colx] - mx) * inv;
+                o.y = __expf(S[(qd + r4 * 4 + 1) * SLD + colx] - mx) * inv;
+                o.z = __expf(S[(qd + r4 * 4 + 2) * SLD + colx] - mx) * inv;
+                o.w = __expf(S[(qd + r4 * 4 + 3) * SLD + colx] - mx) * inv;
+                *(float4*)&PT[(long long)colx * 128 + qd + r4 * 4] = o;
             }
         }
     } else {
@@ -800,12 +708,12 @@
         #pragma unroll
         for (int i = 0; i < 4; i++) {
             #pragma unroll
-            for (int j = 0; j < 4; j++) {
-                const int gnn = bn + wn + j * 16 + lr;
+            for (int j = 0; j < 2; j++) {
+                const int gnn = bn + wc + j * 16 + lr;
                 if (gnn >= N) continue;
                 #pragma unroll
                 for (int r = 0; r < 4; r++) {
-                    const int gm = wm + i * 16 + quad * 4 + r;
+                    const int gm = wr + i * 16 + quad * 4 + r;
                     float v = acc[i][j][r];
                     if (sizes && (gm >= s1 || gnn >= s2)) v = 0.f;
                     if (flags & F_ACCUM) v += C[(long long)gm * ldc + gnn];
@@ -971,28 +879,28 @@
         convert_all<<<dim3(2, 2512), 256, 0, stream>>>(t);
     }
 
-    gemm_proj<<<dim3(5, 512), 256, 0, stream>>>(
+    gemm_proj<<<dim3(5, 512), 512, 0, stream>>>(
         x1, x2, emb, NORMS, W1H, W1L, W2H, W2L, T, FBUF, F1X);
-    gemm_bat<1><<<dim3(1, 1, 2 * BATCH), 256, 0, stream>>>(
+    gemm_bat<1><<<dim3(1, 1, 2 * BATCH), 512, 0, stream>>>(
         FBUF, F1X, FBUF, nullptr, ATT, nullptr,
         SEQ, EDIM, 320, EDIM, EDIM, SEQ, sbF, sbF, sbSS, 0,
         0, bias_intra, nullptr, 1);
-    gemm_xp<<<dim3(2, 1, 2 * BATCH), 256, 0, stream>>>(
+    gemm_xp<<<dim3(2, 1, 2 * BATCH), 512, 0, stream>>>(
         ATT, T, x1, x2, emb, NORMS, WPA1H, WPA1L, WPA2H, WPA2L, X1CAT);
 
-    gemm_flat<1><<<dim3(2, 512), 256, 0, stream>>>(
+    gemm_flat<1><<<dim3(2, 512), 512, 0, stream>>>(
         X1CAT, WAH, WAL, WAH, WAL, 1 << 30, F12, nullptr, nullptr,
         2 * BSTOK, PDIM, 224, 400, 224, PDIM, F_RELU);
-    gemm_bat<2><<<dim3(1, 1, BATCH), 256, 0, stream>>>(
+    gemm_bat<2><<<dim3(1, 1, BATCH), 512, 0, stream>>>(
         F12, nullptr, F2, nullptr, SIMP, SMTP,
         SEQ, PDIM, 224, PDIM, PDIM, SEQ, sbFP, sbFP, sbFP, sbFP,
         0, nullptr, SIZES, 0);
-    gemm_bat<0><<<dim3(2, 1, 2 * BATCH), 256, 0, stream>>>(
+    gemm_bat<0><<<dim3(2, 1, 2 * BATCH), 512, 0, stream>>>(
         SIMP, SMTP, T2, T1, X1CAT + 200, nullptr,
         PDIM, SEQ, SEQ, SEQ, SEQ, 400, sbFP, sbT, sbC, 0,
         0, nullptr, nullptr, 0);
 
-    gemm_flat<3><<<dim3(4, 512), 256, 0, stream>>>(
+    gemm_flat<3><<<dim3(4, 512), 512, 0, stream>>>(
         X1CAT, WC1H, WC1L, WC2H, WC2L, BSTOK,
         nullptr, POOL, SIZES,
         2 * BSTOK, 400, 416, 400, 416, 400, F_RELU);
```

New measurement: 478.4 us. 13.8% less time.
